# Kernel tuning notes

Measured on AMD Instinct MI355X. Metric: run time of the kernel, lower is better.

Reference implementation:

```python
import jax, jax.numpy as jnp
import numpy as np

B, N, D = 4, 4096, 64   # batch, num points, point-feature channels
K = 24                  # original_k_neighbors
GO = 128                # graph_out_channel = max(32, (D*2//8)*8)
MLP = [64, 128, 256]
HALF = MLP[-1] // 2     # graph_feature_mapping out channels
EPS = 1e-5

def leaky(x):
    return jnp.where(x > 0, x, 0.2 * x)

def bn(x, gamma, beta, axes):
    # training-mode batch norm (biased variance, like torch normalization); channel last
    m = jnp.mean(x, axes, keepdims=True)
    v = jnp.var(x, axes, keepdims=True)
    return (x - m) * jax.lax.rsqrt(v + EPS) * gamma + beta

def knn_idx(p, k):
    # p: [B,N,3] -> indices of k nearest neighbors (self excluded), [B,N,k]
    sq = jnp.sum(p * p, -1)
    dist = sq[:, :, None] + sq[:, None, :] - 2.0 * jnp.einsum('bnc,bmc->bnm', p, p)
    _, idx = jax.lax.top_k(-dist, k + 1)   # smallest k+1 distances
    return idx[:, :, 1:]

def setup_inputs():
    key = jax.random.key(0)
    ks = jax.random.split(key, 8)
    w = lambda i, s: jax.random.normal(ks[i], s, jnp.float32) * 0.05
    return {
        'xyz': jax.random.normal(ks[0], (B, 3, N), jnp.float32),
        'points': jax.random.normal(ks[1], (B, D, N), jnp.float32),
        'ec_w': w(2, (GO, 2 * D)),
        'ec_g': jnp.ones((GO,), jnp.float32), 'ec_b': jnp.zeros((GO,), jnp.float32),
        'gm_w': w(3, (HALF, GO)),
        'gm_g': jnp.ones((HALF,), jnp.float32), 'gm_b': jnp.zeros((HALF,), jnp.float32),
        'w0': w(4, (MLP[0], D + 3)), 'bias0': jnp.zeros((MLP[0],), jnp.float32),
        'g0': jnp.ones((MLP[0],), jnp.float32), 'be0': jnp.zeros((MLP[0],), jnp.float32),
        'w1': w(5, (MLP[1], MLP[0])), 'bias1': jnp.zeros((MLP[1],), jnp.float32),
        'g1': jnp.ones((MLP[1],), jnp.float32), 'be1': jnp.zeros((MLP[1],), jnp.float32),
        'w2': w(6, (MLP[2], MLP[1])), 'bias2': jnp.zeros((MLP[2],), jnp.float32),
        'g2': jnp.ones((MLP[2],), jnp.float32), 'be2': jnp.zeros((MLP[2],), jnp.float32),
        'fu_w': w(7, (MLP[2], MLP[2] + HALF)),
        'fu_g': jnp.ones((MLP[2],), jnp.float32), 'fu_b': jnp.zeros((MLP[2],), jnp.float32),
    }

def reference(xyz, points, ec_w, ec_g, ec_b, gm_w, gm_g, gm_b,
              w0, bias0, g0, be0, w1, bias1, g1, be1, w2, bias2, g2, be2,
              fu_w, fu_g, fu_b):
    xyz_t = jnp.transpose(xyz, (0, 2, 1))     # [B,N,3]
    pts_t = jnp.transpose(points, (0, 2, 1))  # [B,N,D]
    edges = knn_idx(xyz_t, K)                 # [B,N,K]
    # --- EdgeConv on original graph ---
    nb = jax.vmap(lambda f, e: f[e])(pts_t, edges)  # gather: [B,N,K,D]
    ctr = pts_t[:, :, None, :]
    ef = jnp.concatenate([jnp.broadcast_to(ctr, nb.shape), nb - ctr], -1)  # [B,N,K,2D]
    h = jnp.einsum('bnkc,oc->bnko', ef, ec_w)
    h = leaky(bn(h, ec_g, ec_b, (0, 1, 2)))
    gfeat = jnp.max(h, axis=2)                # max over neighbors -> [B,N,GO]
    # --- graph_feature_mapping ---
    gm = jnp.einsum('bnc,oc->bno', gfeat, gm_w)
    gm = leaky(bn(gm, gm_g, gm_b, (0, 1)))    # [B,N,HALF]
    # --- group_all PointNet MLP ---
    g = jnp.concatenate([xyz_t, pts_t], -1)   # [B,N,D+3]
    for wl, bl, gl, bel in ((w0, bias0, g0, be0), (w1, bias1, g1, be1), (w2, bias2, g2, be2)):
        g = jax.nn.relu(bn(jnp.einsum('bnc,oc->bno', g, wl) + bl, gl, bel, (0, 1)))
    point_feat = jnp.max(g, axis=1)           # [B, MLP[-1]]
    graph_glob = jnp.max(gm, axis=1)          # [B, HALF]
    # --- fusion ---
    fused = jnp.concatenate([point_feat, graph_glob], -1)
    f = jnp.einsum('bc,oc->bo', fused, fu_w)
    f = leaky(bn(f, fu_g, fu_b, (0,)))
    return f[:, :, None]                      # [B, MLP[-1], 1]
```

## Files before the change

### kernel.cpp

```cpp
#include <hip/hip_runtime.h>

#define NPTS 4096
#define QN   16384
#define KNN  24

static constexpr size_t OFF_EDGES = 0;
static constexpr size_t OFF_BIG   = 393216;
static constexpr size_t OFF_A     = OFF_BIG;
static constexpr size_t OFF_C     = OFF_BIG + 2097152;
static constexpr size_t OFF_M     = OFF_BIG + 4194304;
static constexpr size_t OFF_L0    = OFF_BIG + 6553600;
static constexpr size_t OFF_L1    = OFF_L0 + 1048576;
static constexpr size_t ST_BASE   = OFF_L1 + 2097152;
static constexpr size_t ST_BN1    = ST_BASE;
static constexpr size_t ST_GM     = ST_BASE + 256;
static constexpr size_t ST_L0     = ST_BASE + 512;
static constexpr size_t ST_L1     = ST_BASE + 640;
static constexpr size_t ST_L2     = ST_BASE + 896;
static constexpr size_t RMX_GM    = ST_BASE + 1408;
static constexpr size_t RMN_GM    = ST_BASE + 1920;
static constexpr size_t RMX_L2    = ST_BASE + 2432;
static constexpr size_t RMN_L2    = ST_BASE + 3456;
static constexpr int    ST_COUNT  = 4480;

__device__ inline unsigned fmap(float f) {
    unsigned u = __float_as_uint(f);
    return (u & 0x80000000u) ? ~u : (u | 0x80000000u);
}
__device__ inline float funmap(unsigned u) {
    unsigned v = (u & 0x80000000u) ? (u & 0x7fffffffu) : ~u;
    return __uint_as_float(v);
}

__device__ inline void xcd_decode(int v, int& b, int& t) {
    b = (v & 7) >> 1;
    t = ((v >> 3) << 1) | (v & 1);
}

template<int I, int O, int OH, int MODE, bool HASBIAS, bool WRITE_RAW, bool MINMAX>
__device__ void layer_part(unsigned char* smem, int b, int chunk, int o0,
    const float* __restrict__ inraw, const float* __restrict__ inst, float rcnt,
    const float* __restrict__ ing, const float* __restrict__ inbe,
    const float* __restrict__ W, const float* __restrict__ bias,
    const float* __restrict__ xyz, const float* __restrict__ pts,
    float* __restrict__ outraw, float* __restrict__ outst,
    unsigned* __restrict__ rmax, unsigned* __restrict__ rmin)
{
    constexpr int OP = OH + 4;
    constexpr int OW = OH / 16;
    float* ns  = (float*)smem;
    float* nb  = ns + I;
    float* inl = (float*)(smem + 1024);
    float* wl  = (float*)(smem + 1024 + 17408);
    int q0 = b * 4096 + chunk * 64;

    if (MODE != 0) {
        if (threadIdx.x < I) {
            int c = threadIdx.x;
            float m = inst[c] * rcnt;
            float v = inst[I + c] * rcnt - m * m;
            float inv = 1.0f / sqrtf(v + 1e-5f);
            float sc = inv * ing[c];
            ns[c] = sc;
            nb[c] = inbe[c] - m * sc;
        }
    }

    int ng = threadIdx.x & 15, og = threadIdx.x >> 4;
    float acc[4][OW];
    #pragma unroll
    for (int r = 0; r < 4; ++r)
        #pragma unroll
        for (int i = 0; i < OW; ++i) acc[r][i] = 0.f;

    for (int ct = 0; ct < I; ct += 64) {
        int CT = (I - ct < 64) ? (I - ct) : 64;
        __syncthreads();
        if (MODE == 0) {
            for (int idx = threadIdx.x; idx < CT * 64; idx += 256) {
                int c = idx >> 6, p = idx & 63;
                int ch = ct + c;
                float v = (ch < 3) ? xyz[((size_t)(b * 3 + ch) << 12) + chunk * 64 + p]
                                   : pts[((size_t)(b * 64 + ch - 3) << 12) + chunk * 64 + p];
                inl[c * 68 + p] = v;
            }
        } else {
            const float* src = inraw + (size_t)q0 * I + ct;
            #pragma unroll
            for (int it = 0; it < 4; ++it) {
                int idx = threadIdx.x + it * 256;
                int c = idx & 63, pq = idx >> 6;
                float sc_ = ns[ct + c], sh_ = nb[ct + c];
                float4 v;
                v.x = fmaf(src[(size_t)(pq * 4 + 0) * I + c], sc_, sh_);
                v.y = fmaf(src[(size_t)(pq * 4 + 1) * I + c], sc_, sh_);
                v.z = fmaf(src[(size_t)(pq * 4 + 2) * I + c], sc_, sh_);
                v.w = fmaf(src[(size_t)(pq * 4 + 3) * I + c], sc_, sh_);
                if (MODE == 1) {
                    v.x = fmaxf(v.x, 0.f); v.y = fmaxf(v.y, 0.f);
                    v.z = fmaxf(v.z, 0.f); v.w = fmaxf(v.w, 0.f);
                } else {
                    v.x = (v.x > 0.f) ? v.x : 0.2f * v.x;
                    v.y = (v.y > 0.f) ? v.y : 0.2f * v.y;
                    v.z = (v.z > 0.f) ? v.z : 0.2f * v.z;
                    v.w = (v.w > 0.f) ? v.w : 0.2f * v.w;
                }
                *(float4*)&inl[c * 68 + pq * 4] = v;
            }
        }
        if ((I & 3) == 0) {
            for (int idx = threadIdx.x; idx < (CT / 4) * OH; idx += 256) {
                int cq = idx & 15, o = idx >> 4;
                float4 wv4 = *(const float4*)&W[(size_t)(o0 + o) * I + ct + cq * 4];
                wl[(cq * 4 + 0) * OP + o] = wv4.x;
                wl[(cq * 4 + 1) * OP + o] = wv4.y;
                wl[(cq * 4 + 2) * OP + o] = wv4.z;
                wl[(cq * 4 + 3) * OP + o] = wv4.w;
            }
        } else {
            for (int idx = threadIdx.x; idx < CT * OH; idx += 256) {
                int o = idx / CT, cc = idx - o * CT;
                wl[cc * OP + o] = W[(size_t)(o0 + o) * I + ct + cc];
            }
        }
        __syncthreads();
        for (int cc = 0; cc < CT; ++cc) {
            float4 pv = *(const float4*)&inl[cc * 68 + ng * 4];
            float pvv[4] = {pv.x, pv.y, pv.z, pv.w};
            #pragma unroll
            for (int i4 = 0; i4 < OW / 4; ++i4) {
                float4 wv = *(const float4*)&wl[cc * OP + og * OW + i4 * 4];
                #pragma unroll
                for (int r = 0; r < 4; ++r) {
                    acc[r][i4 * 4 + 0] = fmaf(pvv[r], wv.x, acc[r][i4 * 4 + 0]);
                    acc[r][i4 * 4 + 1] = fmaf(pvv[r], wv.y, acc[r][i4 * 4 + 1]);
                    acc[r][i4 * 4 + 2] = fmaf(pvv[r], wv.z, acc[r][i4 * 4 + 2]);
                    acc[r][i4 * 4 + 3] = fmaf(pvv[r], wv.w, acc[r][i4 * 4 + 3]);
                }
            }
        }
    }

    if (HASBIAS) {
        #pragma unroll
        for (int i = 0; i < OW; ++i) {
            float bv = bias[o0 + og * OW + i];
            #pragma unroll
            for (int r = 0; r < 4; ++r) acc[r][i] += bv;
        }
    }
    __syncthreads();
    #pragma unroll
    for (int r = 0; r < 4; ++r)
        #pragma unroll
        for (int i = 0; i < OW; ++i)
            wl[(ng * 4 + r) * OP + og * OW + i] = acc[r][i];
    __syncthreads();

    if (WRITE_RAW) {
        for (int idx = threadIdx.x; idx < 64 * OH; idx += 256) {
            int p = idx / OH, o = idx - p * OH;
            outraw[(size_t)(q0 + p) * O + o0 + o] = wl[p * OP + o];
        }
    }
    if (threadIdx.x < OH) {
        int o = threadIdx.x;
        float s1 = 0.f, s2 = 0.f;
        float mx = -__builtin_inff(), mn = __builtin_inff();
        #pragma unroll 8
        for (int p = 0; p < 64; ++p) {
            float v = wl[p * OP + o];
            s1 += v;
            s2 = fmaf(v, v, s2);
            if (MINMAX) { mx = fmaxf(mx, v); mn = fminf(mn, v); }
        }
        atomicAdd(&outst[o0 + o], s1);
        atomicAdd(&outst[O + o0 + o], s2);
        if (MINMAX) {
            atomicMax(&rmax[b * O + o0 + o], fmap(mx));
            atomicMin(&rmin[b * O + o0 + o], fmap(mn));
        }
    }
}

__global__ __launch_bounds__(256) void kA(const float* __restrict__ xyz,
                                          const float* __restrict__ pts,
                                          const float* __restrict__ ec_w,
                                          int* __restrict__ edges,
                                          float* __restrict__ afeat,
                                          float* __restrict__ cfeat,
                                          unsigned* __restrict__ stz) {
    __shared__ __align__(16) unsigned char smem[25856];
    int u = blockIdx.x;
    if (u < 4096) {
        float4* cand = (float4*)smem;
        unsigned long long* bufall = (unsigned long long*)(smem + 16384);
        int b = u >> 10;
        int wave = threadIdx.x >> 6, lane = threadIdx.x & 63;
        int n = ((u & 1023) << 2) + wave;
        const float* xb = xyz + (size_t)b * 3 * 4096;
        unsigned long long* wbuf = bufall + wave * 128;

        float xq = xb[n], yq = xb[4096 + n], zq = xb[8192 + n];
        float sqq = __fadd_rn(__fadd_rn(__fmul_rn(xq, xq), __fmul_rn(yq, yq)), __fmul_rn(zq, zq));

        unsigned T = 0xFFFFFFFFu;
        int count = 0;

        auto reduce = [&]() {
            unsigned long long ka = (lane < count) ? wbuf[lane] : ~0ull;
            int ra = 0;
            if (count > 64) {
                unsigned long long kb = (lane + 64 < count) ? wbuf[lane + 64] : ~0ull;
                int rb = 0;
                for (int j = 0; j < count; ++j) {
                    unsigned long long kj = wbuf[j];
                    ra += (kj < ka);
                    rb += (kj < kb);
                }
                if (rb < 25) wbuf[rb] = kb;
            } else {
                for (int j = 0; j < count; ++j) {
                    unsigned long long kj = wbuf[j];
                    ra += (kj < ka);
                }
            }
            if (ra < 25) wbuf[ra] = ka;
            count = 25;
            T = (unsigned)(wbuf[24] >> 32);
        };

        for (int strip = 0; strip < 4; ++strip) {
            __syncthreads();
            for (int i = threadIdx.x; i < 1024; i += 256) {
                int j = strip * 1024 + i;
                float x = xb[j], y = xb[4096 + j], z = xb[8192 + j];
                float sq = __fadd_rn(__fadd_rn(__fmul_rn(x, x), __fmul_rn(y, y)), __fmul_rn(z, z));
                cand[i] = make_float4(x, y, z, sq);
            }
            __syncthreads();
            for (int t = 0; t < 16; ++t) {
                float4 cv = cand[t * 64 + lane];
                float dot = __fadd_rn(__fadd_rn(__fmul_rn(xq, cv.x), __fmul_rn(yq, cv.y)), __fmul_rn(zq, cv.z));
                float d = __fsub_rn(__fadd_rn(sqq, cv.w), __fmul_rn(2.0f, dot));
                unsigned du = fmap(d);
                bool surv = (du <= T);
                unsigned long long m = __ballot(surv);
                if (m) {
                    if (surv) {
                        int ofs = __popcll(m & ((1ull << lane) - 1ull));
                        unsigned idx = (unsigned)(strip * 1024 + t * 64 + lane);
                        wbuf[count + ofs] = ((unsigned long long)du << 32) | idx;
                    }
                    count += (int)__popcll(m);
                    if (count >= 64) reduce();
                }
            }
        }
        reduce();
        if (lane >= 1 && lane < 25)
            edges[((size_t)(b * 4096 + n)) * KNN + lane - 1] = (int)(unsigned)(wbuf[lane] & 0xFFFFFFFFull);
    } else if (u < 6144) {
        int v = u - 4096;
        int b, t;
        xcd_decode(v, b, t);
        int nchunk = t & 63, sub = t >> 6;
        int which = sub >> 2;
        int o0 = (sub & 3) * 32;
        int n0 = nchunk * 64;

        float* inl = (float*)smem;
        float* wl  = (float*)(smem + 16640);
        const float* pb = pts + (size_t)b * 64 * 4096;

        for (int idx = threadIdx.x; idx < 64 * 64; idx += 256) {
            int c = idx >> 6, p = idx & 63;
            inl[p * 65 + c] = pb[(size_t)c * 4096 + n0 + p];
        }
        for (int idx = threadIdx.x; idx < 64 * 32; idx += 256) {
            int cc = idx & 63, o = idx >> 6;
            float w2v = ec_w[(o0 + o) * 128 + 64 + cc];
            wl[cc * 36 + o] = which ? w2v : (ec_w[(o0 + o) * 128 + cc] - w2v);
        }
        __syncthreads();

        int ng = threadIdx.x & 15, og = threadIdx.x >> 4;
        float acc[4][2] = {{0.f, 0.f}, {0.f, 0.f}, {0.f, 0.f}, {0.f, 0.f}};
        for (int cc = 0; cc < 64; ++cc) {
            float pv[4];
            #pragma unroll
            for (int r = 0; r < 4; ++r) pv[r] = inl[(ng * 4 + r) * 65 + cc];
            float2 wv = *(const float2*)&wl[cc * 36 + og * 2];
            #pragma unroll
            for (int r = 0; r < 4; ++r) {
                acc[r][0] = fmaf(pv[r], wv.x, acc[r][0]);
                acc[r][1] = fmaf(pv[r], wv.y, acc[r][1]);
            }
        }
        __syncthreads();
        #pragma unroll
        for (int r = 0; r < 4; ++r) {
            wl[(ng * 4 + r) * 36 + og * 2 + 0] = acc[r][0];
            wl[(ng * 4 + r) * 36 + og * 2 + 1] = acc[r][1];
        }
        __syncthreads();
        float* dst = (which ? cfeat : afeat) + ((size_t)(b * 4096 + n0)) * 128 + o0;
        for (int idx = threadIdx.x; idx < 64 * 32; idx += 256) {
            int p = idx >> 5, o = idx & 31;
            dst[(size_t)p * 128 + o] = wl[p * 36 + o];
        }
    } else {
        for (int i = threadIdx.x; i < ST_COUNT; i += 256) {
            bool sentinel = (i >= (int)(RMN_GM - ST_BASE) && i < (int)(RMX_L2 - ST_BASE)) ||
                            (i >= (int)(RMN_L2 - ST_BASE));
            stz[i] = sentinel ? 0xFFFFFFFFu : 0u;
        }
    }
}

__global__ __launch_bounds__(256) void kB(const float* __restrict__ afeat,
                                          const float* __restrict__ cfeat,
                                          const int* __restrict__ edges,
                                          float* __restrict__ M,
                                          float* __restrict__ stBN1,
                                          const float* __restrict__ xyz,
                                          const float* __restrict__ pts,
                                          const float* __restrict__ w0,
                                          const float* __restrict__ bias0,
                                          float* __restrict__ l0raw,
                                          float* __restrict__ stL0) {
    __shared__ __align__(16) unsigned char smem[35840];
    int u = blockIdx.x;
    if (u < 1024) {
        int* eL = (int*)smem;
        float* red = (float*)(smem + 1536);
        int b, chunk;
        xcd_decode(u, b, chunk);
        int q0 = b * 4096 + chunk * 16;
        for (int idx = threadIdx.x; idx < 16 * KNN; idx += 256) eL[idx] = edges[(size_t)q0 * KNN + idx];
        __syncthreads();

        int m = threadIdx.x & 31;
        int g = threadIdx.x >> 5;
        int bbase = b << 12;
        float s1[4] = {0.f, 0.f, 0.f, 0.f}, s2[4] = {0.f, 0.f, 0.f, 0.f};

        #pragma unroll
        for (int half = 0; half < 2; ++half) {
            int p = g + half * 8;
            int q = q0 + p;
            float mx0 = -__builtin_inff(), mx1 = mx0, mx2 = mx0, mx3 = mx0;
            float sv0 = 0.f, sv1 = 0.f, sv2 = 0.f, sv3 = 0.f;
            float qv0 = 0.f, qv1 = 0.f, qv2 = 0.f, qv3 = 0.f;
            #pragma unroll 8
            for (int k = 0; k < KNN; ++k) {
                int e = eL[p * KNN + k];
                float4 v = *(const float4*)&cfeat[((size_t)(bbase + e) << 7) + m * 4];
                mx0 = fmaxf(mx0, v.x); sv0 += v.x; qv0 = fmaf(v.x, v.x, qv0);
                mx1 = fmaxf(mx1, v.y); sv1 += v.y; qv1 = fmaf(v.y, v.y, qv1);
                mx2 = fmaxf(mx2, v.z); sv2 += v.z; qv2 = fmaf(v.z, v.z, qv2);
                mx3 = fmaxf(mx3, v.w); sv3 += v.w; qv3 = fmaf(v.w, v.w, qv3);
            }
            float4 a = *(const float4*)&afeat[((size_t)q << 7) + m * 4];
            float4 mo = make_float4(a.x + mx0, a.y + mx1, a.z + mx2, a.w + mx3);
            *(float4*)&M[((size_t)q << 7) + m * 4] = mo;
            s1[0] += fmaf(24.f, a.x, sv0); s2[0] += 24.f * a.x * a.x + 2.f * a.x * sv0 + qv0;
            s1[1] += fmaf(24.f, a.y, sv1); s2[1] += 24.f * a.y * a.y + 2.f * a.y * sv1 + qv1;
            s1[2] += fmaf(24.f, a.z, sv2); s2[2] += 24.f * a.z * a.z + 2.f * a.z * sv2 + qv2;
            s1[3] += fmaf(24.f, a.w, sv3); s2[3] += 24.f * a.w * a.w + 2.f * a.w * sv3 + qv3;
        }
        #pragma unroll
        for (int j = 0; j < 4; ++j) red[g * 132 + m * 4 + j] = s1[j];
        __syncthreads();
        if (threadIdx.x < 128) {
            float t = 0.f;
            #pragma unroll
            for (int gg = 0; gg < 8; ++gg) t += red[gg * 132 + threadIdx.x];
            atomicAdd(&stBN1[threadIdx.x], t);
        }
        __syncthreads();
        #pragma unroll
        for (int j = 0; j < 4; ++j) red[g * 132 + m * 4 + j] = s2[j];
        __syncthreads();
        if (threadIdx.x < 128) {
            float t = 0.f;
            #pragma unroll
            for (int gg = 0; gg < 8; ++gg) t += red[gg * 132 + threadIdx.x];
            atomicAdd(&stBN1[128 + threadIdx.x], t);
        }
    } else {
        int v = u - 1024;
        int b, chunk;
        xcd_decode(v, b, chunk);
        layer_part<67, 64, 64, 0, true, true, false>(smem, b, chunk, 0,
            nullptr, nullptr, 0.f, nullptr, nullptr,
            w0, bias0, xyz, pts, l0raw, stL0, nullptr, nullptr);
    }
}

__global__ __launch_bounds__(256) void kC(const float* __restrict__ M,
                                          const float* __restrict__ stBN1,
                                          const float* __restrict__ ec_g,
                                          const float* __restrict__ ec_b,
                                          const float* __restrict__ gm_w,
                                          float* __restrict__ stGM,
                                          unsigned* __restrict__ rmxGM,
                                          unsigned* __restrict__ rmnGM,
                                          const float* __restrict__ l0raw,
                                          const float* __restrict__ stL0,
                                          const float* __restrict__ g0,
                                          const float* __restrict__ be0,
                                          const float* __restrict__ w1,
                                          const float* __restrict__ bias1,
                                          float* __restrict__ l1raw,
                                          float* __restrict__ stL1) {
    __shared__ __align__(16) unsigned char smem[52224];
    int u = blockIdx.x;
    if (u < 256) {
        int b, chunk;
        xcd_decode(u, b, chunk);
        layer_part<128, 128, 128, 2, false, false, true>(smem, b, chunk, 0,
            M, stBN1, 1.0f / 393216.0f, ec_g, ec_b,
            gm_w, nullptr, nullptr, nullptr, nullptr, stGM, rmxGM, rmnGM);
    } else {
        int v = u - 256;
        int b, chunk;
        xcd_decode(v, b, chunk);
        layer_part<64, 128, 128, 1, true, true, false>(smem, b, chunk, 0,
            l0raw, stL0, 1.0f / 16384.0f, g0, be0,
            w1, bias1, nullptr, nullptr, l1raw, stL1, nullptr, nullptr);
    }
}

__global__ __launch_bounds__(256) void kD(const float* __restrict__ l1raw,
                                          const float* __restrict__ stL1,
                                          const float* __restrict__ g1,
                                          const float* __restrict__ be1,
                                          const float* __restrict__ w2,
                                          const float* __restrict__ bias2,
                                          float* __restrict__ stL2,
                                          unsigned* __restrict__ rmxL2,
                                          unsigned* __restrict__ rmnL2) {
    __shared__ __align__(16) unsigned char smem[52224];
    int u = blockIdx.x;
    int b, t;
    xcd_decode(u, b, t);
    int chunk = t & 63, y = t >> 6;
    layer_part<128, 256, 128, 1, true, false, true>(smem, b, chunk, y * 128,
        l1raw, stL1, 1.0f / 16384.0f, g1, be1,
        w2, bias2, nullptr, nullptr, nullptr, stL2, rmxL2, rmnL2);
}

__global__ __launch_bounds__(256) void kE(const float* __restrict__ stGM,
                                          const float* __restrict__ gm_g,
                                          const float* __restrict__ gm_b,
                                          const unsigned* __restrict__ rmxGM,
                                          const unsigned* __restrict__ rmnGM,
                                          const float* __restrict__ stL2,
                                          const float* __restrict__ g2,
                                          const float* __restrict__ be2,
                                          const unsigned* __restrict__ rmxL2,
                                          const unsigned* __restrict__ rmnL2,
                                          const float* __restrict__ fu_w,
                                          const float* __restrict__ fu_g,
                                          const float* __restrict__ fu_b,
                                          float* __restrict__ out) {
    __shared__ float fl[4 * 384];
    const float rc = 1.0f / 16384.0f;
    int t = threadIdx.x;
    {
        int o = t;
        float m = stL2[o] * rc;
        float v = stL2[256 + o] * rc - m * m;
        float sc = g2[o] / sqrtf(v + 1e-5f);
        float sh = be2[o] - m * sc;
        #pragma unroll
        for (int b = 0; b < 4; ++b) {
            float f1 = fmaxf(fmaf(funmap(rmxL2[b * 256 + o]), sc, sh), 0.f);
            float f2 = fmaxf(fmaf(funmap(rmnL2[b * 256 + o]), sc, sh), 0.f);
            fl[b * 384 + o] = fmaxf(f1, f2);
        }
    }
    if (t < 128) {
        int o = t;
        float m = stGM[o] * rc;
        float v = stGM[128 + o] * rc - m * m;
        float sc = gm_g[o] / sqrtf(v + 1e-5f);
        float sh = gm_b[o] - m * sc;
        #pragma unroll
        for (int b = 0; b < 4; ++b) {
            float x1 = fmaf(funmap(rmxGM[b * 128 + o]), sc, sh);
            x1 = (x1 > 0.f) ? x1 : 0.2f * x1;
            float x2 = fmaf(funmap(rmnGM[b * 128 + o]), sc, sh);
            x2 = (x2 > 0.f) ? x2 : 0.2f * x2;
            fl[b * 384 + 256 + o] = fmaxf(x1, x2);
        }
    }
    __syncthreads();
    int o = t;
    float f[4];
    #pragma unroll
    for (int bb = 0; bb < 4; ++bb) {
        float acc = 0.f;
        for (int c = 0; c < 384; ++c) acc = fmaf(fl[bb * 384 + c], fu_w[(size_t)o * 384 + c], acc);
        f[bb] = acc;
    }
    float m = 0.25f * (f[0] + f[1] + f[2] + f[3]);
    float var = 0.f;
    #pragma unroll
    for (int bb = 0; bb < 4; ++bb) { float tt = f[bb] - m; var = fmaf(tt, tt, var); }
    var *= 0.25f;
    float inv = 1.0f / sqrtf(var + 1e-5f);
    float gv = fu_g[o], bv = fu_b[o];
    #pragma unroll
    for (int bb = 0; bb < 4; ++bb) {
        float xx = (f[bb] - m) * inv * gv + bv;
        xx = (xx > 0.0f) ? xx : 0.2f * xx;
        out[bb * 256 + o] = xx;
    }
}

extern "C" void kernel_launch(void* const* d_in, const int* in_sizes, int n_in,
                              void* d_out, int out_size, void* d_ws, size_t ws_size,
                              hipStream_t stream) {
    const float* xyz   = (const float*)d_in[0];
    const float* pts   = (const float*)d_in[1];
    const float* ec_w  = (const float*)d_in[2];
    const float* ec_g  = (const float*)d_in[3];
    const float* ec_b  = (const float*)d_in[4];
    const float* gm_w  = (const float*)d_in[5];
    const float* gm_g  = (const float*)d_in[6];
    const float* gm_b  = (const float*)d_in[7];
    const float* w0    = (const float*)d_in[8];
    const float* bias0 = (const float*)d_in[9];
    const float* g0    = (const float*)d_in[10];
    const float* be0   = (const float*)d_in[11];
    const float* w1    = (const float*)d_in[12];
    const float* bias1 = (const float*)d_in[13];
    const float* g1    = (const float*)d_in[14];
    const float* be1   = (const float*)d_in[15];
    const float* w2    = (const float*)d_in[16];
    const float* bias2 = (const float*)d_in[17];
    const float* g2    = (const float*)d_in[18];
    const float* be2   = (const float*)d_in[19];
    const float* fu_w  = (const float*)d_in[20];
    const float* fu_g  = (const float*)d_in[21];
    const float* fu_b  = (const float*)d_in[22];

    float* ws = (float*)d_ws;
    float* out = (float*)d_out;

    kA<<<6145, 256, 0, stream>>>(xyz, pts, ec_w, (int*)(ws + OFF_EDGES),
                                 ws + OFF_A, ws + OFF_C, (unsigned*)(ws + ST_BASE));
    kB<<<1280, 256, 0, stream>>>(ws + OFF_A, ws + OFF_C, (int*)(ws + OFF_EDGES),
                                 ws + OFF_M, ws + ST_BN1,
                                 xyz, pts, w0, bias0, ws + OFF_L0, ws + ST_L0);
    kC<<<512, 256, 0, stream>>>(ws + OFF_M, ws + ST_BN1, ec_g, ec_b, gm_w,
                                ws + ST_GM, (unsigned*)(ws + RMX_GM), (unsigned*)(ws + RMN_GM),
                                ws + OFF_L0, ws + ST_L0, g0, be0, w1, bias1,
                                ws + OFF_L1, ws + ST_L1);
    kD<<<512, 256, 0, stream>>>(ws + OFF_L1, ws + ST_L1, g1, be1, w2, bias2,
                                ws + ST_L2, (unsigned*)(ws + RMX_L2), (unsigned*)(ws + RMN_L2));
    kE<<<1, 256, 0, stream>>>(ws + ST_GM, gm_g, gm_b,
                              (unsigned*)(ws + RMX_GM), (unsigned*)(ws + RMN_GM),
                              ws + ST_L2, g2, be2,
                              (unsigned*)(ws + RMX_L2), (unsigned*)(ws + RMN_L2),
                              fu_w, fu_g, fu_b, out);
}
```

Baseline: 320.4 us.

## Fuse later stages into one cooperative kernel with grid syncs and wider tiles

Replaces the kB/kC/kD/kE kernel chain with a single persistent cooperative kernel that separates the phases with grid-wide syncs. Layer0 of the PointNet MLP moves into kA, and the later MLP layers use a new 128x128 register-tiled GEMM with 8x8 accumulators per thread. The intent is to cut launch gaps and the long serial tail of the final single-block kernel, and to raise per-thread reuse. The risks are grid.sync overhead, occupancy limits from the larger register tile, and a fixed grid size that may leave the GPU underused.

```diff
diff --git a/kernel.cpp b/kernel.cpp
--- a/kernel.cpp
+++ b/kernel.cpp
@@ -1,4 +1,7 @@
 #include <hip/hip_runtime.h>
+#include <hip/hip_cooperative_groups.h>
+
+namespace cg = cooperative_groups;
 
 #define NPTS 4096
 #define QN   16384
@@ -37,166 +40,25 @@
     t = ((v >> 3) << 1) | (v & 1);
 }
 
-template<int I, int O, int OH, int MODE, bool HASBIAS, bool WRITE_RAW, bool MINMAX>
-__device__ void layer_part(unsigned char* smem, int b, int chunk, int o0,
-    const float* __restrict__ inraw, const float* __restrict__ inst, float rcnt,
-    const float* __restrict__ ing, const float* __restrict__ inbe,
-    const float* __restrict__ W, const float* __restrict__ bias,
-    const float* __restrict__ xyz, const float* __restrict__ pts,
-    float* __restrict__ outraw, float* __restrict__ outst,
-    unsigned* __restrict__ rmax, unsigned* __restrict__ rmin)
-{
-    constexpr int OP = OH + 4;
-    constexpr int OW = OH / 16;
-    float* ns  = (float*)smem;
-    float* nb  = ns + I;
-    float* inl = (float*)(smem + 1024);
-    float* wl  = (float*)(smem + 1024 + 17408);
-    int q0 = b * 4096 + chunk * 64;
-
-    if (MODE != 0) {
-        if (threadIdx.x < I) {
-            int c = threadIdx.x;
-            float m = inst[c] * rcnt;
-            float v = inst[I + c] * rcnt - m * m;
-            float inv = 1.0f / sqrtf(v + 1e-5f);
-            float sc = inv * ing[c];
-            ns[c] = sc;
-            nb[c] = inbe[c] - m * sc;
-        }
-    }
-
-    int ng = threadIdx.x & 15, og = threadIdx.x >> 4;
-    float acc[4][OW];
-    #pragma unroll
-    for (int r = 0; r < 4; ++r)
-        #pragma unroll
-        for (int i = 0; i < OW; ++i) acc[r][i] = 0.f;
-
-    for (int ct = 0; ct < I; ct += 64) {
-        int CT = (I - ct < 64) ? (I - ct) : 64;
-        __syncthreads();
-        if (MODE == 0) {
-            for (int idx = threadIdx.x; idx < CT * 64; idx += 256) {
-                int c = idx >> 6, p = idx & 63;
-                int ch = ct + c;
-                float v = (ch < 3) ? xyz[((size_t)(b * 3 + ch) << 12) + chunk * 64 + p]
-                                   : pts[((size_t)(b * 64 + ch - 3) << 12) + chunk * 64 + p];
-                inl[c * 68 + p] = v;
-            }
-        } else {
-            const float* src = inraw + (size_t)q0 * I + ct;
-            #pragma unroll
-            for (int it = 0; it < 4; ++it) {
-                int idx = threadIdx.x + it * 256;
-                int c = idx & 63, pq = idx >> 6;
-                float sc_ = ns[ct + c], sh_ = nb[ct + c];
-                float4 v;
-                v.x = fmaf(src[(size_t)(pq * 4 + 0) * I + c], sc_, sh_);
-                v.y = fmaf(src[(size_t)(pq * 4 + 1) * I + c], sc_, sh_);
-                v.z = fmaf(src[(size_t)(pq * 4 + 2) * I + c], sc_, sh_);
-                v.w = fmaf(src[(size_t)(pq * 4 + 3) * I + c], sc_, sh_);
-                if (MODE == 1) {
-                    v.x = fmaxf(v.x, 0.f); v.y = fmaxf(v.y, 0.f);
-                    v.z = fmaxf(v.z, 0.f); v.w = fmaxf(v.w, 0.f);
-                } else {
-                    v.x = (v.x > 0.f) ? v.x : 0.2f * v.x;
-                    v.y = (v.y > 0.f) ? v.y : 0.2f * v.y;
-                    v.z = (v.z > 0.f) ? v.z : 0.2f * v.z;
-                    v.w = (v.w > 0.f) ? v.w : 0.2f * v.w;
-                }
-                *(float4*)&inl[c * 68 + pq * 4] = v;
-            }
-        }
-        if ((I & 3) == 0) {
-            for (int idx = threadIdx.x; idx < (CT / 4) * OH; idx += 256) {
-                int cq = idx & 15, o = idx >> 4;
-                float4 wv4 = *(const float4*)&W[(size_t)(o0 + o) * I + ct + cq * 4];
-                wl[(cq * 4 + 0) * OP + o] = wv4.x;
-                wl[(cq * 4 + 1) * OP + o] = wv4.y;
-                wl[(cq * 4 + 2) * OP + o] = wv4.z;
-                wl[(cq * 4 + 3) * OP + o] = wv4.w;
-            }
-        } else {
-            for (int idx = threadIdx.x; idx < CT * OH; idx += 256) {
-                int o = idx / CT, cc = idx - o * CT;
-                wl[cc * OP + o] = W[(size_t)(o0 + o) * I + ct + cc];
-            }
-        }
-        __syncthreads();
-        for (int cc = 0; cc < CT; ++cc) {
-            float4 pv = *(const float4*)&inl[cc * 68 + ng * 4];
-            float pvv[4] = {pv.x, pv.y, pv.z, pv.w};
-            #pragma unroll
-            for (int i4 = 0; i4 < OW / 4; ++i4) {
-                float4 wv = *(const float4*)&wl[cc * OP + og * OW + i4 * 4];
-                #pragma unroll
-                for (int r = 0; r < 4; ++r) {
-                    acc[r][i4 * 4 + 0] = fmaf(pvv[r], wv.x, acc[r][i4 * 4 + 0]);
-                    acc[r][i4 * 4 + 1] = fmaf(pvv[r], wv.y, acc[r][i4 * 4 + 1]);
-                    acc[r][i4 * 4 + 2] = fmaf(pvv[r], wv.z, acc[r][i4 * 4 + 2]);
-                    acc[r][i4 * 4 + 3] = fmaf(pvv[r], wv.w, acc[r][i4 * 4 + 3]);
-                }
-            }
-        }
-    }
-
-    if (HASBIAS) {
-        #pragma unroll
-        for (int i = 0; i < OW; ++i) {
-            float bv = bias[o0 + og * OW + i];
-            #pragma unroll
-            for (int r = 0; r < 4; ++r) acc[r][i] += bv;
-        }
-    }
-    __syncthreads();
-    #pragma unroll
-    for (int r = 0; r < 4; ++r)
-        #pragma unroll
-        for (int i = 0; i < OW; ++i)
-            wl[(ng * 4 + r) * OP + og * OW + i] = acc[r][i];
-    __syncthreads();
-
-    if (WRITE_RAW) {
-        for (int idx = threadIdx.x; idx < 64 * OH; idx += 256) {
-            int p = idx / OH, o = idx - p * OH;
-            outraw[(size_t)(q0 + p) * O + o0 + o] = wl[p * OP + o];
-        }
-    }
-    if (threadIdx.x < OH) {
-        int o = threadIdx.x;
-        float s1 = 0.f, s2 = 0.f;
-        float mx = -__builtin_inff(), mn = __builtin_inff();
-        #pragma unroll 8
-        for (int p = 0; p < 64; ++p) {
-            float v = wl[p * OP + o];
-            s1 += v;
-            s2 = fmaf(v, v, s2);
-            if (MINMAX) { mx = fmaxf(mx, v); mn = fminf(mn, v); }
-        }
-        atomicAdd(&outst[o0 + o], s1);
-        atomicAdd(&outst[O + o0 + o], s2);
-        if (MINMAX) {
-            atomicMax(&rmax[b * O + o0 + o], fmap(mx));
-            atomicMin(&rmin[b * O + o0 + o], fmap(mn));
-        }
-    }
-}
-
 __global__ __launch_bounds__(256) void kA(const float* __restrict__ xyz,
                                           const float* __restrict__ pts,
                                           const float* __restrict__ ec_w,
+                                          const float* __restrict__ w0,
+                                          const float* __restrict__ bias0,
                                           int* __restrict__ edges,
                                           float* __restrict__ afeat,
                                           float* __restrict__ cfeat,
+                                          float* __restrict__ l0raw,
+                                          float* __restrict__ stL0,
                                           unsigned* __restrict__ stz) {
     __shared__ __align__(16) unsigned char smem[25856];
     int u = blockIdx.x;
+    int tid = threadIdx.x;
     if (u < 4096) {
         float4* cand = (float4*)smem;
         unsigned long long* bufall = (unsigned long long*)(smem + 16384);
         int b = u >> 10;
-        int wave = threadIdx.x >> 6, lane = threadIdx.x & 63;
+        int wave = tid >> 6, lane = tid & 63;
         int n = ((u & 1023) << 2) + wave;
         const float* xb = xyz + (size_t)b * 3 * 4096;
         unsigned long long* wbuf = bufall + wave * 128;
@@ -232,7 +94,7 @@
 
         for (int strip = 0; strip < 4; ++strip) {
             __syncthreads();
-            for (int i = threadIdx.x; i < 1024; i += 256) {
+            for (int i = tid; i < 1024; i += 256) {
                 int j = strip * 1024 + i;
                 float x = xb[j], y = xb[4096 + j], z = xb[8192 + j];
                 float sq = __fadd_rn(__fadd_rn(__fmul_rn(x, x), __fmul_rn(y, y)), __fmul_rn(z, z));
@@ -273,18 +135,18 @@
         float* wl  = (float*)(smem + 16640);
         const float* pb = pts + (size_t)b * 64 * 4096;
 
-        for (int idx = threadIdx.x; idx < 64 * 64; idx += 256) {
+        for (int idx = tid; idx < 64 * 64; idx += 256) {
             int c = idx >> 6, p = idx & 63;
             inl[p * 65 + c] = pb[(size_t)c * 4096 + n0 + p];
         }
-        for (int idx = threadIdx.x; idx < 64 * 32; idx += 256) {
+        for (int idx = tid; idx < 64 * 32; idx += 256) {
             int cc = idx & 63, o = idx >> 6;
             float w2v = ec_w[(o0 + o) * 128 + 64 + cc];
             wl[cc * 36 + o] = which ? w2v : (ec_w[(o0 + o) * 128 + cc] - w2v);
         }
         __syncthreads();
 
-        int ng = threadIdx.x & 15, og = threadIdx.x >> 4;
+        int ng = tid & 15, og = tid >> 4;
         float acc[4][2] = {{0.f, 0.f}, {0.f, 0.f}, {0.f, 0.f}, {0.f, 0.f}};
         for (int cc = 0; cc < 64; ++cc) {
             float pv[4];
@@ -305,12 +167,85 @@
         }
         __syncthreads();
         float* dst = (which ? cfeat : afeat) + ((size_t)(b * 4096 + n0)) * 128 + o0;
-        for (int idx = threadIdx.x; idx < 64 * 32; idx += 256) {
+        for (int idx = tid; idx < 64 * 32; idx += 256) {
             int p = idx >> 5, o = idx & 31;
             dst[(size_t)p * 128 + o] = wl[p * 36 + o];
         }
+    } else if (u < 6400) {
+        int v = u - 6144;
+        int b, chunk;
+        xcd_decode(v, b, chunk);
+        int n0 = chunk * 64;
+        int q0 = b * 4096 + n0;
+        float* inl = (float*)smem;
+        float* wl  = (float*)(smem + 8704);
+        int ng = tid & 15, og = tid >> 4;
+        float acc[4][4] = {};
+
+        for (int ct = 0; ct < 67; ct += 32) {
+            int CT = (67 - ct < 32) ? (67 - ct) : 32;
+            __syncthreads();
+            for (int idx = tid; idx < CT * 16; idx += 256) {
+                int p4 = idx & 15, c = idx >> 4;
+                int ch = ct + c;
+                const float* srow = (ch < 3) ? &xyz[((size_t)(b * 3 + ch) << 12) + n0]
+                                             : &pts[((size_t)(b * 64 + ch - 3) << 12) + n0];
+                float4 v4;
+                v4.x = srow[p4 * 4 + 0];
+                v4.y = srow[p4 * 4 + 1];
+                v4.z = srow[p4 * 4 + 2];
+                v4.w = srow[p4 * 4 + 3];
+                *(float4*)&inl[c * 68 + p4 * 4] = v4;
+            }
+            for (int idx = tid; idx < CT * 64; idx += 256) {
+                int o = idx & 63, cc = idx >> 6;
+                wl[cc * 68 + o] = w0[o * 67 + ct + cc];
+            }
+            __syncthreads();
+            for (int cc = 0; cc < CT; ++cc) {
+                float4 pv = *(const float4*)&inl[cc * 68 + ng * 4];
+                float4 wv = *(const float4*)&wl[cc * 68 + og * 4];
+                float pvv[4] = {pv.x, pv.y, pv.z, pv.w};
+                float wvv[4] = {wv.x, wv.y, wv.z, wv.w};
+                #pragma unroll
+                for (int r = 0; r < 4; ++r)
+                    #pragma unroll
+                    for (int k = 0; k < 4; ++k)
+                        acc[r][k] = fmaf(pvv[r], wvv[k], acc[r][k]);
+            }
+        }
+        #pragma unroll
+        for (int k = 0; k < 4; ++k) {
+            float bv = bias0[og * 4 + k];
+            #pragma unroll
+            for (int r = 0; r < 4; ++r) acc[r][k] += bv;
+        }
+        __syncthreads();
+        float* st = inl;
+        #pragma unroll
+        for (int r = 0; r < 4; ++r)
+            #pragma unroll
+            for (int k = 0; k < 4; ++k)
+                st[(ng * 4 + r) * 68 + og * 4 + k] = acc[r][k];
+        __syncthreads();
+        for (int idx = tid; idx < 1024; idx += 256) {
+            int p = idx >> 4, o4 = (idx & 15) * 4;
+            *(float4*)&l0raw[(size_t)(q0 + p) * 64 + o4] = *(const float4*)&st[p * 68 + o4];
+        }
+        if (tid < 64) {
+            float s1 = 0.f, s2 = 0.f;
+            #pragma unroll 8
+            for (int p = 0; p < 64; ++p) {
+                float vv = st[p * 68 + tid];
+                s1 += vv;
+                s2 = fmaf(vv, vv, s2);
+            }
+            atomicAdd(&stL0[tid], s1);
+            atomicAdd(&stL0[64 + tid], s2);
+        }
     } else {
-        for (int i = threadIdx.x; i < ST_COUNT; i += 256) {
+        for (int i = tid; i < ST_COUNT; i += 256) {
+            if (i >= 512 && i < 640) continue;
             bool sentinel = (i >= (int)(RMN_GM - ST_BASE) && i < (int)(RMX_L2 - ST_BASE)) ||
                             (i >= (int)(RMN_L2 - ST_BASE));
             stz[i] = sentinel ? 0xFFFFFFFFu : 0u;
@@ -318,52 +253,214 @@
     }
 }
 
-__global__ __launch_bounds__(256) void kB(const float* __restrict__ afeat,
-                                          const float* __restrict__ cfeat,
-                                          const int* __restrict__ edges,
-                                          float* __restrict__ M,
-                                          float* __restrict__ stBN1,
-                                          const float* __restrict__ xyz,
-                                          const float* __restrict__ pts,
-                                          const float* __restrict__ w0,
-                                          const float* __restrict__ bias0,
-                                          float* __restrict__ l0raw,
-                                          float* __restrict__ stL0) {
-    __shared__ __align__(16) unsigned char smem[35840];
-    int u = blockIdx.x;
-    if (u < 1024) {
+template<int I, int TO, int MODE, bool RAW, bool MINMAX>
+__device__ void layer128(unsigned char* smem, int b, int chunk, int o0,
+    const float* __restrict__ inraw, const float* __restrict__ inst, float rcnt,
+    const float* __restrict__ ing, const float* __restrict__ inbe,
+    const float* __restrict__ W, const float* __restrict__ bias,
+    float* __restrict__ outraw, float* __restrict__ outst,
+    unsigned* __restrict__ rmax, unsigned* __restrict__ rmin)
+{
+    float* ns  = (float*)smem;
+    float* nb  = ns + 128;
+    float* inl = (float*)(smem + 1024);
+    float* wl  = (float*)(smem + 1024 + 16896);
+    int tid = threadIdx.x;
+    int ng = tid & 15, og = tid >> 4;
+    int q0 = b * 4096 + chunk * 128;
+
+    if (tid < I) {
+        float m = inst[tid] * rcnt;
+        float v = inst[I + tid] * rcnt - m * m;
+        float sc = ing[tid] / sqrtf(v + 1e-5f);
+        ns[tid] = sc;
+        nb[tid] = inbe[tid] - m * sc;
+    }
+
+    float acc[8][8] = {};
+    for (int ct = 0; ct < I; ct += 32) {
+        __syncthreads();
+        const float* src = inraw + (size_t)q0 * I + ct;
+        #pragma unroll
+        for (int it = 0; it < 4; ++it) {
+            int idx = tid + it * 256;
+            int c = idx & 31, p4 = idx >> 5;
+            float sc_ = ns[ct + c], sh_ = nb[ct + c];
+            float4 v;
+            v.x = fmaf(src[(size_t)(p4 * 4 + 0) * I + c], sc_, sh_);
+            v.y = fmaf(src[(size_t)(p4 * 4 + 1) * I + c], sc_, sh_);
+            v.z = fmaf(src[(size_t)(p4 * 4 + 2) * I + c], sc_, sh_);
+            v.w = fmaf(src[(size_t)(p4 * 4 + 3) * I + c], sc_, sh_);
+            if (MODE == 1) {
+                v.x = fmaxf(v.x, 0.f); v.y = fmaxf(v.y, 0.f);
+                v.z = fmaxf(v.z, 0.f); v.w = fmaxf(v.w, 0.f);
+            } else {
+                v.x = (v.x > 0.f) ? v.x : 0.2f * v.x;
+                v.y = (v.y > 0.f) ? v.y : 0.2f * v.y;
+                v.z = (v.z > 0.f) ? v.z : 0.2f * v.z;
+                v.w = (v.w > 0.f) ? v.w : 0.2f * v.w;
+            }
+            *(float4*)&inl[c * 132 + p4 * 4] = v;
+        }
+        #pragma unroll
+        for (int it = 0; it < 4; ++it) {
+            int idx = tid + it * 256;
+            int o = idx & 127, c4 = idx >> 7;
+            float4 w4 = *(const float4*)&W[(size_t)(o0 + o) * I + ct + c4 * 4];
+            wl[(c4 * 4 + 0) * 132 + o] = w4.x;
+            wl[(c4 * 4 + 1) * 132 + o] = w4.y;
+            wl[(c4 * 4 + 2) * 132 + o] = w4.z;
+            wl[(c4 * 4 + 3) * 132 + o] = w4.w;
+        }
+        __syncthreads();
+        for (int cc = 0; cc < 32; ++cc) {
+            float4 pl = *(const float4*)&inl[cc * 132 + ng * 4];
+            float4 ph = *(const float4*)&inl[cc * 132 + 64 + ng * 4];
+            float4 wo = *(const float4*)&wl[cc * 132 + og * 4];
+            float4 wh = *(const float4*)&wl[cc * 132 + 64 + og * 4];
+            float pv[8] = {pl.x, pl.y, pl.z, pl.w, ph.x, ph.y, ph.z, ph.w};
+            float wv[8] = {wo.x, wo.y, wo.z, wo.w, wh.x, wh.y, wh.z, wh.w};
+            #pragma unroll
+            for (int r = 0; r < 8; ++r)
+                #pragma unroll
+                for (int k = 0; k < 8; ++k)
+                    acc[r][k] = fmaf(pv[r], wv[k], acc[r][k]);
+        }
+    }
+
+    if (bias != nullptr) {
+        #pragma unroll
+        for (int k = 0; k < 8; ++k) {
+            int o = (k < 4) ? (og * 4 + k) : (64 + og * 4 + k - 4);
+            float bv = bias[o0 + o];
+            #pragma unroll
+            for (int r = 0; r < 8; ++r) acc[r][k] += bv;
+        }
+    }
+
+    if (RAW) {
+        float* st = (float*)(smem + 1024);
+        #pragma unroll
+        for (int h = 0; h < 2; ++h) {
+            __syncthreads();
+            #pragma unroll
+            for (int r = 0; r < 8; ++r) {
+                int p = (r < 4) ? (ng * 4 + r) : (64 + ng * 4 + r - 4);
+                #pragma unroll
+                for (int k = 0; k < 4; ++k)
+                    st[p * 68 + og * 4 + k] = acc[r][h * 4 + k];
+            }
+            __syncthreads();
+            for (int idx = tid; idx < 2048; idx += 256) {
+                int p = idx >> 4, o4 = (idx & 15) * 4;
+                *(float4*)&outraw[(size_t)(q0 + p) * TO + h * 64 + o4] = *(const float4*)&st[p * 68 + o4];
+            }
+            if (tid < 64) {
+                float s1 = 0.f, s2 = 0.f;
+                #pragma unroll 8
+                for (int p = 0; p < 128; ++p) {
+                    float vv = st[p * 68 + tid];
+                    s1 += vv;
+                    s2 = fmaf(vv, vv, s2);
+                }
+                atomicAdd(&outst[h * 64 + tid], s1);
+                atomicAdd(&outst[TO + h * 64 + tid], s2);
+            }
+        }
+    } else {
+        float* red = (float*)(smem + 1024);
+        __syncthreads();
+        #pragma unroll
+        for (int k = 0; k < 8; ++k) {
+            int o = (k < 4) ? (og * 4 + k) : (64 + og * 4 + k - 4);
+            float s1 = 0.f, s2 = 0.f;
+            float mx = -__builtin_inff(), mn = __builtin_inff();
+            #pragma unroll
+            for (int r = 0; r < 8; ++r) {
+                float vv = acc[r][k];
+                s1 += vv;
+                s2 = fmaf(vv, vv, s2);
+                mx = fmaxf(mx, vv);
+                mn = fminf(mn, vv);
+            }
+            *(float4*)&red[(o * 17 + ng) * 4] = make_float4(s1, s2, mx, mn);
+        }
+        __syncthreads();
+        if (tid < 128) {
+            float s1 = 0.f, s2 = 0.f;
+            float mx = -__builtin_inff(), mn = __builtin_inff();
+            #pragma unroll
+            for (int g2 = 0; g2 < 16; ++g2) {
+                float4 t4 = *(const float4*)&red[(tid * 17 + g2) * 4];
+                s1 += t4.x;
+                s2 += t4.y;
+                mx = fmaxf(mx, t4.z);
+                mn = fminf(mn, t4.w);
+            }
+            atomicAdd(&outst[o0 + tid], s1);
+            atomicAdd(&outst[TO + o0 + tid], s2);
+            if (MINMAX) {
+                atomicMax(&rmax[b * TO + o0 + tid], fmap(mx));
+                atomicMin(&rmin[b * TO + o0 + tid], fmap(mn));
+            }
+        }
+    }
+}
+
+struct P2 {
+    const float* afeat; const float* cfeat; const int* edges;
+    float* M; float* stBN1;
+    const float* ec_g; const float* ec_b; const float* gm_w;
+    float* stGM; unsigned* rmxGM; unsigned* rmnGM;
+    const float* l0raw; const float* stL0; const float* g0; const float* be0;
+    const float* w1; const float* bias1; float* l1raw; float* stL1;
+    const float* g1; const float* be1; const float* w2; const float* bias2;
+    float* stL2; unsigned* rmxL2; unsigned* rmnL2;
+    const float* gm_g; const float* gm_b; const float* g2; const float* be2;
+    const float* fu_w; const float* fu_g; const float* fu_b; float* out;
+};
+
+__global__ __launch_bounds__(256, 4) void kFused(P2 p) {
+    __shared__ __align__(16) unsigned char smem[36864];
+    cg::grid_group grid = cg::this_grid();
+    int bid = blockIdx.x;
+    int gsz = gridDim.x;
+    int tid = threadIdx.x;
+
+    for (int u = bid; u < 1024; u += gsz) {
         int* eL = (int*)smem;
         float* red = (float*)(smem + 1536);
         int b, chunk;
         xcd_decode(u, b, chunk);
         int q0 = b * 4096 + chunk * 16;
-        for (int idx = threadIdx.x; idx < 16 * KNN; idx += 256) eL[idx] = edges[(size_t)q0 * KNN + idx];
-        __syncthreads();
-
-        int m = threadIdx.x & 31;
-        int g = threadIdx.x >> 5;
+        __syncthreads();
+        for (int idx = tid; idx < 16 * KNN; idx += 256) eL[idx] = p.edges[(size_t)q0 * KNN + idx];
+        __syncthreads();
+
+        int m = tid & 31;
+        int g = tid >> 5;
         int bbase = b << 12;
         float s1[4] = {0.f, 0.f, 0.f, 0.f}, s2[4] = {0.f, 0.f, 0.f, 0.f};
 
         #pragma unroll
         for (int half = 0; half < 2; ++half) {
-            int p = g + half * 8;
-            int q = q0 + p;
+            int pp = g + half * 8;
+            int q = q0 + pp;
             float mx0 = -__builtin_inff(), mx1 = mx0, mx2 = mx0, mx3 = mx0;
             float sv0 = 0.f, sv1 = 0.f, sv2 = 0.f, sv3 = 0.f;
             float qv0 = 0.f, qv1 = 0.f, qv2 = 0.f, qv3 = 0.f;
             #pragma unroll 8
             for (int k = 0; k < KNN; ++k) {
-                int e = eL[p * KNN + k];
-                float4 v = *(const float4*)&cfeat[((size_t)(bbase + e) << 7) + m * 4];
+                int e = eL[pp * KNN + k];
+                float4 v = *(const float4*)&p.cfeat[((size_t)(bbase + e) << 7) + m * 4];
                 mx0 = fmaxf(mx0, v.x); sv0 += v.x; qv0 = fmaf(v.x, v.x, qv0);
                 mx1 = fmaxf(mx1, v.y); sv1 += v.y; qv1 = fmaf(v.y, v.y, qv1);
                 mx2 = fmaxf(mx2, v.z); sv2 += v.z; qv2 = fmaf(v.z, v.z, qv2);
                 mx3 = fmaxf(mx3, v.w); sv3 += v.w; qv3 = fmaf(v.w, v.w, qv3);
             }
-            float4 a = *(const float4*)&afeat[((size_t)q << 7) + m * 4];
+            float4 a = *(const float4*)&p.afeat[((size_t)q << 7) + m * 4];
             float4 mo = make_float4(a.x + mx0, a.y + mx1, a.z + mx2, a.w + mx3);
-            *(float4*)&M[((size_t)q << 7) + m * 4] = mo;
+            *(float4*)&p.M[((size_t)q << 7) + m * 4] = mo;
             s1[0] += fmaf(24.f, a.x, sv0); s2[0] += 24.f * a.x * a.x + 2.f * a.x * sv0 + qv0;
             s1[1] += fmaf(24.f, a.y, sv1); s2[1] += 24.f * a.y * a.y + 2.f * a.y * sv1 + qv1;
             s1[2] += fmaf(24.f, a.z, sv2); s2[2] += 24.f * a.z * a.z + 2.f * a.z * sv2 + qv2;
@@ -372,151 +469,105 @@
         #pragma unroll
         for (int j = 0; j < 4; ++j) red[g * 132 + m * 4 + j] = s1[j];
         __syncthreads();
-        if (threadIdx.x < 128) {
+        if (tid < 128) {
             float t = 0.f;
             #pragma unroll
-            for (int gg = 0; gg < 8; ++gg) t += red[gg * 132 + threadIdx.x];
-            atomicAdd(&stBN1[threadIdx.x], t);
+            for (int gg = 0; gg < 8; ++gg) t += red[gg * 132 + tid];
+            atomicAdd(&p.stBN1[tid], t);
         }
         __syncthreads();
         #pragma unroll
         for (int j = 0; j < 4; ++j) red[g * 132 + m * 4 + j] = s2[j];
         __syncthreads();
-        if (threadIdx.x < 128) {
+        if (tid < 128) {
             float t = 0.f;
             #pragma unroll
-            for (int gg = 0; gg < 8; ++gg) t += red[gg * 132 + threadIdx.x];
-            atomicAdd(&stBN1[128 + threadIdx.x], t);
-        }
-    } else {
-        int v = u - 1024;
+            for (int gg = 0; gg < 8; ++gg) t += red[gg * 132 + tid];
+            atomicAdd(&p.stBN1[128 + tid], t);
+        }
+    }
+    grid.sync();
+
+    for (int u = bid; u < 256; u += gsz) {
+        if (u < 128) {
+            int b, chunk;
+            xcd_decode(u, b, chunk);
+            layer128<128, 128, 2, false, true>(smem, b, chunk, 0,
+                p.M, p.stBN1, 1.0f / 393216.0f, p.ec_g, p.ec_b,
+                p.gm_w, nullptr, nullptr, p.stGM, p.rmxGM, p.rmnGM);
+        } else {
+            int b, chunk;
+            xcd_decode(u - 128, b, chunk);
+            layer128<64, 128, 1, true, false>(smem, b, chunk, 0,
+                p.l0raw, p.stL0, 1.0f / 16384.0f, p.g0, p.be0,
+                p.w1, p.bias1, p.l1raw, p.stL1, nullptr, nullptr);
+        }
+    }
+    grid.sync();
+
+    for (int u = bid; u < 256; u += gsz) {
+        int half = u >> 7;
         int b, chunk;
-        xcd_decode(v, b, chunk);
-        layer_part<67, 64, 64, 0, true, true, false>(smem, b, chunk, 0,
-            nullptr, nullptr, 0.f, nullptr, nullptr,
-            w0, bias0, xyz, pts, l0raw, stL0, nullptr, nullptr);
-    }
-}
-
-__global__ __launch_bounds__(256) void kC(const float* __restrict__ M,
-                                          const float* __restrict__ stBN1,
-                                          const float* __restrict__ ec_g,
-                                          const float* __restrict__ ec_b,
-                                          const float* __restrict__ gm_w,
-                                          float* __restrict__ stGM,
-                                          unsigned* __restrict__ rmxGM,
-                                          unsigned* __restrict__ rmnGM,
-                                          const float* __restrict__ l0raw,
-                                          const float* __restrict__ stL0,
-                                          const float* __restrict__ g0,
-                                          const float* __restrict__ be0,
-                                          const float* __restrict__ w1,
-                                          const float* __restrict__ bias1,
-                                          float* __restrict__ l1raw,
-                                          float* __restrict__ stL1) {
-    __shared__ __align__(16) unsigned char smem[52224];
-    int u = blockIdx.x;
-    if (u < 256) {
-        int b, chunk;
-        xcd_decode(u, b, chunk);
-        layer_part<128, 128, 128, 2, false, false, true>(smem, b, chunk, 0,
-            M, stBN1, 1.0f / 393216.0f, ec_g, ec_b,
-            gm_w, nullptr, nullptr, nullptr, nullptr, stGM, rmxGM, rmnGM);
-    } else {
-        int v = u - 256;
-        int b, chunk;
-        xcd_decode(v, b, chunk);
-        layer_part<64, 128, 128, 1, true, true, false>(smem, b, chunk, 0,
-            l0raw, stL0, 1.0f / 16384.0f, g0, be0,
-            w1, bias1, nullptr, nullptr, l1raw, stL1, nullptr, nullptr);
-    }
-}
-
-__global__ __launch_bounds__(256) void kD(const float* __restrict__ l1raw,
-                                          const float* __restrict__ stL1,
-                                          const float* __restrict__ g1,
-                                          const float* __restrict__ be1,
-                                          const float* __restrict__ w2,
-                                          const float* __restrict__ bias2,
-                                          float* __restrict__ stL2,
-                                          unsigned* __restrict__ rmxL2,
-                                          unsigned* __restrict__ rmnL2) {
-    __shared__ __align__(16) unsigned char smem[52224];
-    int u = blockIdx.x;
-    int b, t;
-    xcd_decode(u, b, t);
-    int chunk = t & 63, y = t >> 6;
-    layer_part<128, 256, 128, 1, true, false, true>(smem, b, chunk, y * 128,
-        l1raw, stL1, 1.0f / 16384.0f, g1, be1,
-        w2, bias2, nullptr, nullptr, nullptr, stL2, rmxL2, rmnL2);
-}
-
-__global__ __launch_bounds__(256) void kE(const float* __restrict__ stGM,
-                                          const float* __restrict__ gm_g,
-                                          const float* __restrict__ gm_b,
-                                          const unsigned* __restrict__ rmxGM,
-                                          const unsigned* __restrict__ rmnGM,
-                                          const float* __restrict__ stL2,
-                                          const float* __restrict__ g2,
-                                          const float* __restrict__ be2,
-                                          const unsigned* __restrict__ rmxL2,
-                                          const unsigned* __restrict__ rmnL2,
-                                          const float* __restrict__ fu_w,
-                                          const float* __restrict__ fu_g,
-                                          const float* __restrict__ fu_b,
-                                          float* __restrict__ out) {
-    __shared__ float fl[4 * 384];
-    const float rc = 1.0f / 16384.0f;
-    int t = threadIdx.x;
-    {
-        int o = t;
-        float m = stL2[o] * rc;
-        float v = stL2[256 + o] * rc - m * m;
-        float sc = g2[o] / sqrtf(v + 1e-5f);
-        float sh = be2[o] - m * sc;
-        #pragma unroll
-        for (int b = 0; b < 4; ++b) {
-            float f1 = fmaxf(fmaf(funmap(rmxL2[b * 256 + o]), sc, sh), 0.f);
-            float f2 = fmaxf(fmaf(funmap(rmnL2[b * 256 + o]), sc, sh), 0.f);
-            fl[b * 384 + o] = fmaxf(f1, f2);
-        }
-    }
-    if (t < 128) {
-        int o = t;
-        float m = stGM[o] * rc;
-        float v = stGM[128 + o] * rc - m * m;
-        float sc = gm_g[o] / sqrtf(v + 1e-5f);
-        float sh = gm_b[o] - m * sc;
-        #pragma unroll
-        for (int b = 0; b < 4; ++b) {
-            float x1 = fmaf(funmap(rmxGM[b * 128 + o]), sc, sh);
-            x1 = (x1 > 0.f) ? x1 : 0.2f * x1;
-            float x2 = fmaf(funmap(rmnGM[b * 128 + o]), sc, sh);
-            x2 = (x2 > 0.f) ? x2 : 0.2f * x2;
-            fl[b * 384 + 256 + o] = fmaxf(x1, x2);
-        }
-    }
-    __syncthreads();
-    int o = t;
-    float f[4];
-    #pragma unroll
-    for (int bb = 0; bb < 4; ++bb) {
-        float acc = 0.f;
-        for (int c = 0; c < 384; ++c) acc = fmaf(fl[bb * 384 + c], fu_w[(size_t)o * 384 + c], acc);
-        f[bb] = acc;
-    }
-    float m = 0.25f * (f[0] + f[1] + f[2] + f[3]);
-    float var = 0.f;
-    #pragma unroll
-    for (int bb = 0; bb < 4; ++bb) { float tt = f[bb] - m; var = fmaf(tt, tt, var); }
-    var *= 0.25f;
-    float inv = 1.0f / sqrtf(var + 1e-5f);
-    float gv = fu_g[o], bv = fu_b[o];
-    #pragma unroll
-    for (int bb = 0; bb < 4; ++bb) {
-        float xx = (f[bb] - m) * inv * gv + bv;
-        xx = (xx > 0.0f) ? xx : 0.2f * xx;
-        out[bb * 256 + o] = xx;
+        xcd_decode(u & 127, b, chunk);
+        layer128<128, 256, 1, false, true>(smem, b, chunk, half * 128,
+            p.l1raw, p.stL1, 1.0f / 16384.0f, p.g1, p.be1,
+            p.w2, p.bias2, nullptr, p.stL2, p.rmxL2, p.rmnL2);
+    }
+    grid.sync();
+
+    if (bid == 0) {
+        float* fl = (float*)smem;
+        const float rc = 1.0f / 16384.0f;
+        {
+            int o = tid;
+            float m = p.stL2[o] * rc;
+            float v = p.stL2[256 + o] * rc - m * m;
+            float sc = p.g2[o] / sqrtf(v + 1e-5f);
+            float sh = p.be2[o] - m * sc;
+            #pragma unroll
+            for (int b = 0; b < 4; ++b) {
+                float f1 = fmaxf(fmaf(funmap(p.rmxL2[b * 256 + o]), sc, sh), 0.f);
+                float f2 = fmaxf(fmaf(funmap(p.rmnL2[b * 256 + o]), sc, sh), 0.f);
+                fl[b * 384 + o] = fmaxf(f1, f2);
+            }
+        }
+        if (tid < 128) {
+            int o = tid;
+            float m = p.stGM[o] * rc;
+            float v = p.stGM[128 + o] * rc - m * m;
+            float sc = p.gm_g[o] / sqrtf(v + 1e-5f);
+            float sh = p.gm_b[o] - m * sc;
+            #pragma unroll
+            for (int b = 0; b < 4; ++b) {
+                float x1 = fmaf(funmap(p.rmxGM[b * 128 + o]), sc, sh);
+                x1 = (x1 > 0.f) ? x1 : 0.2f * x1;
+                float x2 = fmaf(funmap(p.rmnGM[b * 128 + o]), sc, sh);
+                x2 = (x2 > 0.f) ? x2 : 0.2f * x2;
+                fl[b * 384 + 256 + o] = fmaxf(x1, x2);
+            }
+        }
+        __syncthreads();
+        int o = tid;
+        float f[4];
+        #pragma unroll
+        for (int bb = 0; bb < 4; ++bb) {
+            float acc = 0.f;
+            for (int c = 0; c < 384; ++c) acc = fmaf(fl[bb * 384 + c], p.fu_w[(size_t)o * 384 + c], acc);
+            f[bb] = acc;
+        }
+        float m = 0.25f * (f[0] + f[1] + f[2] + f[3]);
+        float var = 0.f;
+        #pragma unroll
+        for (int bb = 0; bb < 4; ++bb) { float tt = f[bb] - m; var = fmaf(tt, tt, var); }
+        var *= 0.25f;
+        float inv = 1.0f / sqrtf(var + 1e-5f);
+        float gv = p.fu_g[o], bv = p.fu_b[o];
+        #pragma unroll
+        for (int bb = 0; bb < 4; ++bb) {
+            float xx = (f[bb] - m) * inv * gv + bv;
+            xx = (xx > 0.0f) ? xx : 0.2f * xx;
+            p.out[bb * 256 + o] = xx;
+        }
     }
 }
 
@@ -550,20 +601,29 @@
     float* ws = (float*)d_ws;
     float* out = (float*)d_out;
 
-    kA<<<6145, 256, 0, stream>>>(xyz, pts, ec_w, (int*)(ws + OFF_EDGES),
-                                 ws + OFF_A, ws + OFF_C, (unsigned*)(ws + ST_BASE));
-    kB<<<1280, 256, 0, stream>>>(ws + OFF_A, ws + OFF_C, (int*)(ws + OFF_EDGES),
-                                 ws + OFF_M, ws + ST_BN1,
-                                 xyz, pts, w0, bias0, ws + OFF_L0, ws + ST_L0);
-    kC<<<512, 256, 0, stream>>>(ws + OFF_M, ws + ST_BN1, ec_g, ec_b, gm_w,
-                                ws + ST_GM, (unsigned*)(ws + RMX_GM), (unsigned*)(ws + RMN_GM),
-                                ws + OFF_L0, ws + ST_L0, g0, be0, w1, bias1,
-                                ws + OFF_L1, ws + ST_L1);
-    kD<<<512, 256, 0, stream>>>(ws + OFF_L1, ws + ST_L1, g1, be1, w2, bias2,
-                                ws + ST_L2, (unsigned*)(ws + RMX_L2), (unsigned*)(ws + RMN_L2));
-    kE<<<1, 256, 0, stream>>>(ws + ST_GM, gm_g, gm_b,
-                              (unsigned*)(ws + RMX_GM), (unsigned*)(ws + RMN_GM),
-                              ws + ST_L2, g2, be2,
-                              (unsigned*)(ws + RMX_L2), (unsigned*)(ws + RMN_L2),
-                              fu_w, fu_g, fu_b, out);
+    hipMemsetAsync(ws + ST_L0, 0, 128 * sizeof(float), stream);
+
+    kA<<<6401, 256, 0, stream>>>(xyz, pts, ec_w, w0, bias0,
+                                 (int*)(ws + OFF_EDGES), ws + OFF_A, ws + OFF_C,
+                                 ws + OFF_L0, ws + ST_L0, (unsigned*)(ws + ST_BASE));
+
+    P2 p2;
+    p2.afeat = ws + OFF_A;  p2.cfeat = ws + OFF_C;  p2.edges = (const int*)(ws + OFF_EDGES);
+    p2.M = ws + OFF_M;      p2.stBN1 = ws + ST_BN1;
+    p2.ec_g = ec_g;         p2.ec_b = ec_b;          p2.gm_w = gm_w;
+    p2.stGM = ws + ST_GM;   p2.rmxGM = (unsigned*)(ws + RMX_GM); p2.rmnGM = (unsigned*)(ws + RMN_GM);
+    p2.l0raw = ws + OFF_L0; p2.stL0 = ws + ST_L0;    p2.g0 = g0;  p2.be0 = be0;
+    p2.w1 = w1;             p2.bias1 = bias1;        p2.l1raw = ws + OFF_L1; p2.stL1 = ws + ST_L1;
+    p2.g1 = g1;             p2.be1 = be1;            p2.w2 = w2;  p2.bias2 = bias2;
+    p2.stL2 = ws + ST_L2;   p2.rmxL2 = (unsigned*)(ws + RMX_L2); p2.rmnL2 = (unsigned*)(ws + RMN_L2);
+    p2.gm_g = gm_g;         p2.gm_b = gm_b;          p2.g2 = g2;  p2.be2 = be2;
+    p2.fu_w = fu_w;         p2.fu_g = fu_g;          p2.fu_b = fu_b; p2.out = out;
+
+    void* args[] = {&p2};
+    int maxB = 0;
+    hipOccupancyMaxActiveBlocksPerMultiprocessor(&maxB, (const void*)kFused, 256, 0);
+    if (maxB < 1) maxB = 1;
+    int grid = maxB * 256;
+    if (grid > 1024) grid = 1024;
+    hipLaunchCooperativeKernel((const void*)kFused, dim3(grid), dim3(256), args, 0, stream);
 }
```

Result: slower. 563.8 us (+76.0%).
